# Optimization experiments

Measured on AMD Instinct MI355X. Metric: run time of the kernel, lower is better.

The kernel has to match this reference:

```python
import jax, jax.numpy as jnp
import numpy as np

H = 4096          # hidden_size
I = 11008         # intermediate_size
G = 128           # AWQ group_size
# AWQ interleaved nibble order within each packed int32
_ORDER = jnp.array([0, 4, 1, 5, 2, 6, 3, 7], dtype=jnp.int32) * 4


def _mk_lin(key, K, N):
    k1, k2, k3 = jax.random.split(key, 3)
    qw = jax.random.randint(k1, (K, N // 8), 0, 100, dtype=jnp.int32)
    qz = jax.random.randint(k2, (K // G, N // 8), 0, 100, dtype=jnp.int32)
    sc = jax.random.normal(k3, (K // G, N), dtype=jnp.float32) * 0.02
    return qw, qz, sc


def setup_inputs() -> dict:
    key = jax.random.key(0)
    ks = jax.random.split(key, 7)
    x = jax.random.normal(ks[0], (8, 16, H), dtype=jnp.float32)
    ln1_w = jnp.ones((H,), dtype=jnp.float32)
    ln2_w = jnp.ones((H,), dtype=jnp.float32)
    qkv_qw, qkv_qz, qkv_sc = _mk_lin(ks[1], H, 3 * H)
    o_qw, o_qz, o_sc = _mk_lin(ks[2], H, H)
    gu_qw, gu_qz, gu_sc = _mk_lin(ks[3], H, 2 * I)
    dn_qw, dn_qz, dn_sc = _mk_lin(ks[4], I, H)
    return dict(x=x, ln1_w=ln1_w, ln2_w=ln2_w,
                qkv_qw=qkv_qw, qkv_qz=qkv_qz, qkv_sc=qkv_sc,
                o_qw=o_qw, o_qz=o_qz, o_sc=o_sc,
                gu_qw=gu_qw, gu_qz=gu_qz, gu_sc=gu_sc,
                dn_qw=dn_qw, dn_qz=dn_qz, dn_sc=dn_sc)


def rmsnorm(x, w, eps=1e-6):
    return x * jax.lax.rsqrt(jnp.mean(x * x, axis=-1, keepdims=True) + eps) * w


def dequant(qw, qz, sc):
    # qw: [K, N//8] int32 -> [K, N]; qz: [K//G, N//8] -> [K//G, N]
    K = qw.shape[0]
    N = sc.shape[1]
    w = ((qw[:, :, None] >> _ORDER) & 0xF).reshape(K, N).astype(sc.dtype)
    z = ((qz[:, :, None] >> _ORDER) & 0xF).reshape(K // G, N).astype(sc.dtype)
    return (w - jnp.repeat(z, G, axis=0)) * jnp.repeat(sc, G, axis=0)


def lite_linear(x, qw, qz, sc):
    return x @ dequant(qw, qz, sc)


def reference(x, ln1_w, ln2_w,
              qkv_qw, qkv_qz, qkv_sc,
              o_qw, o_qz, o_sc,
              gu_qw, gu_qz, gu_sc,
              dn_qw, dn_qz, dn_sc):
    residual = x
    h = rmsnorm(x, ln1_w)
    h = lite_linear(h, qkv_qw, qkv_qz, qkv_sc)[..., :H]  # mock attn: take q slice
    h = lite_linear(h, o_qw, o_qz, o_sc)
    h = residual + h
    residual = h
    h = rmsnorm(h, ln2_w)
    gate_up = lite_linear(h, gu_qw, gu_qz, gu_sc)
    gate, up = gate_up[..., :I], gate_up[..., I:]
    h = lite_linear(jax.nn.silu(gate) * up, dn_qw, dn_qz, dn_sc)
    return residual + h
```

## Files before the change

kernel.cpp:

```cpp
#include <hip/hip_runtime.h>

typedef unsigned int   u32;
typedef unsigned short u16;

typedef _Float16 h2  __attribute__((ext_vector_type(2)));
typedef _Float16 h8  __attribute__((ext_vector_type(8)));
typedef float    f32x4 __attribute__((ext_vector_type(4)));

#define M_TOK 128

__device__ __forceinline__ u16 f2h_(float f) {
    _Float16 h = (_Float16)f; return __builtin_bit_cast(u16, h);
}
__device__ __forceinline__ float h2f_(u16 b) {
    _Float16 h = __builtin_bit_cast(_Float16, b); return (float)h;
}
__device__ __forceinline__ void acc8(uint4 v, float* s) {
#pragma unroll
    for (int i = 0; i < 4; ++i) {
        u32 w = ((const u32*)&v)[i];
        s[2 * i]     += h2f_((u16)(w & 0xFFFF));
        s[2 * i + 1] += h2f_((u16)(w >> 16));
    }
}

__constant__ int SHC[8] = {0, 16, 4, 20, 8, 24, 12, 28};

__launch_bounds__(256)
__global__ void pack_zs(const int* __restrict__ qz, const float* __restrict__ sc,
                        u32* __restrict__ zs, int qws, int scs, int Ncols, int total) {
    const int idx = blockIdx.x * 256 + threadIdx.x;
    if (idx >= total) return;
    const int g = idx / Ncols, n = idx - g * Ncols;
    const u32 d = (u32)qz[(size_t)g * qws + (n >> 3)];
    const u32 zj = (d >> SHC[n & 7]) & 15u;
    const u32 mz = 0xE400u | zj;
    const u16 sh = f2h_(sc[(size_t)g * scs + n]);
    zs[(size_t)g * Ncols + n] = mz | ((u32)sh << 16);
}


__launch_bounds__(256)
__global__ void rmsnorm_k(const float* __restrict__ in, const float* __restrict__ w,
                          u16* __restrict__ out) {
    const int row = blockIdx.x;
    const float* x = in + (size_t)row * 4096;
    float ss = 0.f;
#pragma unroll
    for (int j = 0; j < 16; ++j) {
        float v = x[threadIdx.x + 256 * j];
        ss += v * v;
    }
#pragma unroll
    for (int off = 32; off > 0; off >>= 1) ss += __shfl_down(ss, off, 64);
    __shared__ float ws4[4];
    if ((threadIdx.x & 63) == 0) ws4[threadIdx.x >> 6] = ss;
    __syncthreads();
    float total = ws4[0] + ws4[1] + ws4[2] + ws4[3];
    float r = rsqrtf(total * (1.f / 4096.f) + 1e-6f);
    const int mt = row >> 4, l16 = row & 15;
#pragma unroll
    for (int c2 = 0; c2 < 2; ++c2) {
        int c = threadIdx.x * 2 + c2;
        int kb = c >> 2, qq = c & 3;
        u16 o8[8];
#pragma unroll
        for (int j = 0; j < 8; ++j) {
            int i = c * 8 + j;
            o8[j] = f2h_(x[i] * r * w[i]);
        }
        *(uint4*)(out + ((size_t)(kb * 8 + mt) * 64 + qq * 16 + l16) * 8) = *(const uint4*)o8;
    }
}

template<int MSPLIT>
__launch_bounds__(256, MSPLIT == 2 ? 4 : 3)
__global__ void gemm_awq(const u16* __restrict__ A, const u32* __restrict__ zs,
                         const int* __restrict__ qw, u16* __restrict__ part,
                         int qws, int N, int K, int kchunk) {
    constexpr int MT = (MSPLIT == 2) ? 4 : 8;
    __shared__ __align__(16) char ldsB[4 * 9216];

    const int tid = threadIdx.x, w = tid >> 6, lane = tid & 63;
    const int q = lane >> 4, l16 = lane & 15;
    const int mh = (MSPLIT == 2) ? (w >> 1) : 0;
    const int nwg = gridDim.x, bid = blockIdx.x;
    const int qq8 = nwg >> 3, r8 = nwg & 7, xcd = bid & 7, boff = bid >> 3;
    const int bx = (xcd < r8 ? xcd * (qq8 + 1) : r8 * (qq8 + 1) + (xcd - r8) * qq8) + boff;
    const int n0w = (MSPLIT == 2) ? (bx * 64 + (w & 1) * 32) : (bx * 128 + w * 32);
    const int pc0 = n0w >> 3;
    const int kp = lane & 31, h = lane >> 5;
    const int sk = blockIdx.y, kc0 = sk * kchunk, kend = min(kc0 + kchunk, K);

    char* buf0 = ldsB + w * 9216;
    char* buf1 = buf0 + 4608;
    const u16* Ala = A + lane * 8;
    const int* qws_base = qw + pc0;
    const u32* zsA = zs + n0w + h * 8;
    const u32* zsB = zs + n0w + 16 + h * 8;

    f32x4 acc[MT][2] = {};
    uint4 za0, za1, zb0, zb1;

    auto ldraw = [&](int k0) -> uint4 {
        return *(const uint4*)(qws_base + (size_t)(k0 + lane) * qws);
    };
    auto loadzs = [&](int g) {
        za0 = *(const uint4*)(zsA + (size_t)g * N);
        za1 = *(const uint4*)(zsA + (size_t)g * N + 4);
        zb0 = *(const uint4*)(zsB + (size_t)g * N);
        zb1 = *(const uint4*)(zsB + (size_t)g * N + 4);
    };
    auto bperm8 = [&](uint4 rv, int* b) {
        const int i0 = kp * 8, i1 = i0 + 4;
        b[0] = __builtin_amdgcn_ds_bpermute(i0, (int)rv.x);
        b[1] = __builtin_amdgcn_ds_bpermute(i0, (int)rv.y);
        b[2] = __builtin_amdgcn_ds_bpermute(i0, (int)rv.z);
        b[3] = __builtin_amdgcn_ds_bpermute(i0, (int)rv.w);
        b[4] = __builtin_amdgcn_ds_bpermute(i1, (int)rv.x);
        b[5] = __builtin_amdgcn_ds_bpermute(i1, (int)rv.y);
        b[6] = __builtin_amdgcn_ds_bpermute(i1, (int)rv.z);
        b[7] = __builtin_amdgcn_ds_bpermute(i1, (int)rv.w);
    };
    auto emit_all = [&](const int* b, char* buf) {
        u32 qd0 = (u32)(h ? b[1] : b[0]);
        u32 qd1 = (u32)(h ? b[5] : b[4]);
        u32 qd2 = (u32)(h ? b[3] : b[2]);
        u32 qd3 = (u32)(h ? b[7] : b[6]);
        auto emit8 = [&](u32 w0, u32 w1, int nb, uint4 z0, uint4 z1) {
            char* bb = buf + kp * 4 + nb * 144;
            u32 w0s = w0 >> 4, w1s = w1 >> 4;
            auto em = [&](int j, u32 a0, u32 a1, int bsel, u32 zsj) {
                h2 mz = __builtin_bit_cast(h2, __builtin_amdgcn_perm(zsj, zsj, 0x01000100u));
                h2 s2 = __builtin_bit_cast(h2, __builtin_amdgcn_perm(zsj, zsj, 0x03020302u));
                u32 t = __builtin_amdgcn_perm(a1, a0, (u32)(bsel | ((bsel + 4) << 16)));
                u32 u = (t & 0x000F000Fu) | 0x64006400u;
                h2 v = (__builtin_bit_cast(h2, u) + mz) * s2;
                *(u32*)(bb + j * 144) = __builtin_bit_cast(u32, v);
            };
            em(0, w0, w1, 0, z0.x);  em(4, w0, w1, 1, z1.x);
            em(1, w0, w1, 2, z0.y);  em(5, w0, w1, 3, z1.y);
            em(2, w0s, w1s, 0, z0.z); em(6, w0s, w1s, 1, z1.z);
            em(3, w0s, w1s, 2, z0.w); em(7, w0s, w1s, 3, z1.w);
        };
        emit8(qd0, qd1, h * 8, za0, za1);
        emit8(qd2, qd3, 16 + h * 8, zb0, zb1);
    };

    loadzs(kc0 >> 7);
    uint4 rv0 = ldraw(kc0);
    uint4 rv_n = {0, 0, 0, 0}, rv_nn = {0, 0, 0, 0};
    if (kc0 + 64 < kend)  rv_n  = ldraw(kc0 + 64);
    if (kc0 + 128 < kend) rv_nn = ldraw(kc0 + 128);
    {
        int bp0[8];
        bperm8(rv0, bp0);
        emit_all(bp0, buf0);
    }
    if (((kc0 + 64) & 127) == 0 && kc0 + 64 < kend)
        loadzs((kc0 + 64) >> 7);

    char* cur = buf0; char* nxt = buf1;
    int bp[8];
    for (int k0 = kc0; k0 < kend; k0 += 64) {
        const bool kn1 = (k0 + 64) < kend, kn3 = (k0 + 192) < kend;
        uint4 bv[2][2];
#pragma unroll
        for (int c = 0; c < 2; ++c)
#pragma unroll
            for (int nt = 0; nt < 2; ++nt)
                bv[c][nt] = *(const uint4*)(cur + (nt * 16 + l16) * 144 + c * 64 + q * 16);
        if (kn1) bperm8(rv_n, bp);
        const int kb = k0 >> 5;
        __builtin_amdgcn_s_setprio(1);
#pragma unroll
        for (int c = 0; c < 2; ++c) {
            uint4 afc[MT];
#pragma unroll
            for (int mt = 0; mt < MT; ++mt)
                afc[mt] = *(const uint4*)(Ala + (size_t)((kb + c) * 8 + mh * MT + mt) * 512);
#pragma unroll
            for (int mt = 0; mt < MT; ++mt)
#pragma unroll
                for (int nt = 0; nt < 2; ++nt)
                    acc[mt][nt] = __builtin_amdgcn_mfma_f32_16x16x32_f16(
                        __builtin_bit_cast(h8, afc[mt]),
                        __builtin_bit_cast(h8, bv[c][nt]),
                        acc[mt][nt], 0, 0, 0);
        }
        __builtin_amdgcn_s_setprio(0);
        uint4 rv_f = {0, 0, 0, 0};
        if (kn3) rv_f = ldraw(k0 + 192);
        if (kn1) emit_all(bp, nxt);
        if (((k0 + 128) & 127) == 0 && (k0 + 128) < kend)
            loadzs((k0 + 128) >> 7);
        rv_n = rv_nn; rv_nn = rv_f;
        char* t = cur; cur = nxt; nxt = t;
    }

    u16* pp = part + (size_t)sk * M_TOK * N;
#pragma unroll
    for (int mt = 0; mt < MT; ++mt)
#pragma unroll
        for (int nt = 0; nt < 2; ++nt) {
            const int n = n0w + nt * 16 + l16;
#pragma unroll
            for (int r = 0; r < 4; ++r) {
                const int m = (mh * MT + mt) * 16 + q * 4 + r;
                pp[(size_t)m * N + n] = f2h_(acc[mt][nt][r]);
            }
        }
}

__launch_bounds__(256)
__global__ void reduce_to_afrag(const u16* __restrict__ part, u16* __restrict__ out,
                                int SK) {
    const int idx = blockIdx.x * 256 + threadIdx.x;
    const int m = idx >> 9, c = idx & 511;
    float s[8] = {};
    for (int k = 0; k < SK; ++k)
        acc8(*(const uint4*)(part + (size_t)k * 524288 + (size_t)m * 4096 + c * 8), s);
    const int kb = c >> 2, qq = c & 3, mt = m >> 4, l16 = m & 15;
    u16 o8[8];
#pragma unroll
    for (int j = 0; j < 8; ++j) o8[j] = f2h_(s[j]);
    *(uint4*)(out + ((size_t)(kb * 8 + mt) * 64 + qq * 16 + l16) * 8) = *(const uint4*)o8;
}

__launch_bounds__(256)
__global__ void reduce_add_f32(const u16* __restrict__ part, const float* __restrict__ resin,
                               float* __restrict__ out, int SK) {
    const int idx = blockIdx.x * 256 + threadIdx.x;
    const size_t base = (size_t)idx * 8;
    float s[8];
    *(float4*)&s[0] = *(const float4*)(resin + base);
    *(float4*)&s[4] = *(const float4*)(resin + base + 4);
    for (int k = 0; k < SK; ++k)
        acc8(*(const uint4*)(part + (size_t)k * 524288 + base), s);
    *(float4*)(out + base)     = *(const float4*)&s[0];
    *(float4*)(out + base + 4) = *(const float4*)&s[4];
}

__launch_bounds__(256)
__global__ void silu_mul(const u16* __restrict__ part, u16* __restrict__ act, int SK) {
    const int idx = blockIdx.x * 256 + threadIdx.x;
    const int m = idx / 1376, c = idx - m * 1376;
    const int nb = c * 8;
    float g[8] = {}, u[8] = {};
    for (int k = 0; k < SK; ++k) {
        const size_t base = (size_t)k * 2818048 + (size_t)m * 22016 + nb;
        acc8(*(const uint4*)(part + base), g);
        acc8(*(const uint4*)(part + base + 11008), u);
    }
    const int kb = nb >> 5, qq = (nb >> 3) & 3, mt = m >> 4, l16 = m & 15;
    u16 o8[8];
#pragma unroll
    for (int j = 0; j < 8; ++j) {
        float a = g[j] / (1.f + __expf(-g[j])) * u[j];
        o8[j] = f2h_(a);
    }
    *(uint4*)(act + ((size_t)(kb * 8 + mt) * 64 + qq * 16 + l16) * 8) = *(const uint4*)o8;
}

extern "C" void kernel_launch(void* const* d_in, const int* in_sizes, int n_in,
                              void* d_out, int out_size, void* d_ws, size_t ws_size,
                              hipStream_t stream) {
    const float* x      = (const float*)d_in[0];
    const float* ln1_w  = (const float*)d_in[1];
    const float* ln2_w  = (const float*)d_in[2];
    const int*   qkv_qw = (const int*)d_in[3];
    const int*   qkv_qz = (const int*)d_in[4];
    const float* qkv_sc = (const float*)d_in[5];
    const int*   o_qw   = (const int*)d_in[6];
    const int*   o_qz   = (const int*)d_in[7];
    const float* o_sc   = (const float*)d_in[8];
    const int*   gu_qw  = (const int*)d_in[9];
    const int*   gu_qz  = (const int*)d_in[10];
    const float* gu_sc  = (const float*)d_in[11];
    const int*   dn_qw  = (const int*)d_in[12];
    const int*   dn_qz  = (const int*)d_in[13];
    const float* dn_sc  = (const float*)d_in[14];
    float* out = (float*)d_out;

    char* ws = (char*)d_ws;
    u16*   pbuf = (u16*)(ws);
    u32*   zsb  = (u32*)(ws + 45088768);
    u16*   act  = (u16*)(ws + 47906816);
    float* res2 = (float*)(ws + 50724864);
    u16*   slot = (u16*)(ws + 52822016);

    rmsnorm_k<<<128, 256, 0, stream>>>(x, ln1_w, slot);
    pack_zs<<<512, 256, 0, stream>>>(qkv_qz, qkv_sc, zsb, 1536, 12288, 4096, 131072);

    gemm_awq<2><<<dim3(64, 16), 256, 0, stream>>>(slot, zsb, qkv_qw, pbuf,
                                                  1536, 4096, 4096, 256);
    reduce_to_afrag<<<256, 256, 0, stream>>>(pbuf, slot, 16);
    pack_zs<<<512, 256, 0, stream>>>(o_qz, o_sc, zsb, 512, 4096, 4096, 131072);

    gemm_awq<2><<<dim3(64, 16), 256, 0, stream>>>(slot, zsb, o_qw, pbuf,
                                                  512, 4096, 4096, 256);
    reduce_add_f32<<<256, 256, 0, stream>>>(pbuf, x, res2, 16);

    rmsnorm_k<<<128, 256, 0, stream>>>(res2, ln2_w, slot);
    pack_zs<<<2752, 256, 0, stream>>>(gu_qz, gu_sc, zsb, 2752, 22016, 22016, 704512);

    gemm_awq<1><<<dim3(172, 8), 256, 0, stream>>>(slot, zsb, gu_qw, pbuf,
                                                  2752, 22016, 4096, 512);
    silu_mul<<<688, 256, 0, stream>>>(pbuf, act, 8);
    pack_zs<<<1376, 256, 0, stream>>>(dn_qz, dn_sc, zsb, 512, 4096, 4096, 352256);

    gemm_awq<2><<<dim3(64, 20), 256, 0, stream>>>(act, zsb, dn_qw, pbuf,
                                                  512, 4096, 11008, 576);
    reduce_add_f32<<<256, 256, 0, stream>>>(pbuf, res2, out, 20);
}
```

Before: 318.7 us.

## Stage activation tiles in shared LDS and widen GEMM tiles to 128 columns

The GEMM kernel drops its MSPLIT template. Every wave now computes all 128 token rows over 32 columns, so each block covers 128 output columns. Activation fragments are cooperatively loaded into double-buffered shared LDS once per block rather than read from global by each wave, and block-wide barriers are added. The weight prefetch depth drops from two stages to one. Split-K factors and grid shapes are retuned for every projection. This cuts redundant global activation traffic, at the cost of a per-iteration __syncthreads, more LDS use (which lowers possible occupancy), and more accumulator registers for the small-N layers.

Measured after the change: 287.7 us. 1.11x faster.

```diff
diff --git a/kernel.cpp b/kernel.cpp
--- a/kernel.cpp
+++ b/kernel.cpp
@@ -73,33 +73,33 @@
     }
 }
 
-template<int MSPLIT>
-__launch_bounds__(256, MSPLIT == 2 ? 4 : 3)
+__launch_bounds__(256, 3)
 __global__ void gemm_awq(const u16* __restrict__ A, const u32* __restrict__ zs,
                          const int* __restrict__ qw, u16* __restrict__ part,
                          int qws, int N, int K, int kchunk) {
-    constexpr int MT = (MSPLIT == 2) ? 4 : 8;
-    __shared__ __align__(16) char ldsB[4 * 9216];
+    __shared__ __align__(16) char lds[51200];
 
     const int tid = threadIdx.x, w = tid >> 6, lane = tid & 63;
     const int q = lane >> 4, l16 = lane & 15;
-    const int mh = (MSPLIT == 2) ? (w >> 1) : 0;
     const int nwg = gridDim.x, bid = blockIdx.x;
     const int qq8 = nwg >> 3, r8 = nwg & 7, xcd = bid & 7, boff = bid >> 3;
     const int bx = (xcd < r8 ? xcd * (qq8 + 1) : r8 * (qq8 + 1) + (xcd - r8) * qq8) + boff;
-    const int n0w = (MSPLIT == 2) ? (bx * 64 + (w & 1) * 32) : (bx * 128 + w * 32);
+    const int n0w = bx * 128 + w * 32;
     const int pc0 = n0w >> 3;
     const int kp = lane & 31, h = lane >> 5;
     const int sk = blockIdx.y, kc0 = sk * kchunk, kend = min(kc0 + kchunk, K);
 
-    char* buf0 = ldsB + w * 9216;
-    char* buf1 = buf0 + 4608;
-    const u16* Ala = A + lane * 8;
+    char* ldsA0 = lds;
+    char* ldsA1 = lds + 16384;
+    char* myB   = lds + 32768 + w * 4608;
+    const char* Ab = (const char*)A;
+    const int stoff = w * 4096 + lane * 16;
+    const int aoff  = (q * 16 + l16) * 16;
     const int* qws_base = qw + pc0;
     const u32* zsA = zs + n0w + h * 8;
     const u32* zsB = zs + n0w + 16 + h * 8;
 
-    f32x4 acc[MT][2] = {};
+    f32x4 acc[8][2] = {};
     uint4 za0, za1, zb0, zb1;
 
     auto ldraw = [&](int k0) -> uint4 {
@@ -149,64 +149,102 @@
 
     loadzs(kc0 >> 7);
     uint4 rv0 = ldraw(kc0);
-    uint4 rv_n = {0, 0, 0, 0}, rv_nn = {0, 0, 0, 0};
-    if (kc0 + 64 < kend)  rv_n  = ldraw(kc0 + 64);
-    if (kc0 + 128 < kend) rv_nn = ldraw(kc0 + 128);
+    uint4 rv_n = {0, 0, 0, 0};
+    if (kc0 + 64 < kend) rv_n = ldraw(kc0 + 64);
+    {
+        const char* gs = Ab + (size_t)(kc0 >> 5) * 8192 + stoff;
+        uint4 s0 = *(const uint4*)(gs);
+        uint4 s1 = *(const uint4*)(gs + 1024);
+        uint4 s2 = *(const uint4*)(gs + 2048);
+        uint4 s3 = *(const uint4*)(gs + 3072);
+        *(uint4*)(ldsA0 + stoff)        = s0;
+        *(uint4*)(ldsA0 + stoff + 1024) = s1;
+        *(uint4*)(ldsA0 + stoff + 2048) = s2;
+        *(uint4*)(ldsA0 + stoff + 3072) = s3;
+    }
     {
         int bp0[8];
         bperm8(rv0, bp0);
-        emit_all(bp0, buf0);
+        emit_all(bp0, myB);
     }
     if (((kc0 + 64) & 127) == 0 && kc0 + 64 < kend)
         loadzs((kc0 + 64) >> 7);
-
-    char* cur = buf0; char* nxt = buf1;
+    __syncthreads();
+
+    char* cur = ldsA0; char* nxt = ldsA1;
     int bp[8];
     for (int k0 = kc0; k0 < kend; k0 += 64) {
-        const bool kn1 = (k0 + 64) < kend, kn3 = (k0 + 192) < kend;
-        uint4 bv[2][2];
-#pragma unroll
-        for (int c = 0; c < 2; ++c)
+        const bool kn1 = (k0 + 64) < kend, kn2 = (k0 + 128) < kend;
+        uint4 s0 = {0,0,0,0}, s1 = {0,0,0,0}, s2 = {0,0,0,0}, s3 = {0,0,0,0};
+        if (kn1) {
+            const char* gs = Ab + (size_t)((k0 + 64) >> 5) * 8192 + stoff;
+            s0 = *(const uint4*)(gs);
+            s1 = *(const uint4*)(gs + 1024);
+            s2 = *(const uint4*)(gs + 2048);
+            s3 = *(const uint4*)(gs + 3072);
+        }
+        uint4 rv_f = {0, 0, 0, 0};
+        if (kn2) rv_f = ldraw(k0 + 128);
+        {
+            uint4 bvc[2];
 #pragma unroll
             for (int nt = 0; nt < 2; ++nt)
-                bv[c][nt] = *(const uint4*)(cur + (nt * 16 + l16) * 144 + c * 64 + q * 16);
-        if (kn1) bperm8(rv_n, bp);
-        const int kb = k0 >> 5;
-        __builtin_amdgcn_s_setprio(1);
-#pragma unroll
-        for (int c = 0; c < 2; ++c) {
-            uint4 afc[MT];
-#pragma unroll
-            for (int mt = 0; mt < MT; ++mt)
-                afc[mt] = *(const uint4*)(Ala + (size_t)((kb + c) * 8 + mh * MT + mt) * 512);
-#pragma unroll
-            for (int mt = 0; mt < MT; ++mt)
+                bvc[nt] = *(const uint4*)(myB + (nt * 16 + l16) * 144 + q * 16);
+            uint4 afc[8];
+#pragma unroll
+            for (int mt = 0; mt < 8; ++mt)
+                afc[mt] = *(const uint4*)(cur + mt * 1024 + aoff);
+            if (kn1) bperm8(rv_n, bp);
+#pragma unroll
+            for (int mt = 0; mt < 8; ++mt)
 #pragma unroll
                 for (int nt = 0; nt < 2; ++nt)
                     acc[mt][nt] = __builtin_amdgcn_mfma_f32_16x16x32_f16(
                         __builtin_bit_cast(h8, afc[mt]),
-                        __builtin_bit_cast(h8, bv[c][nt]),
+                        __builtin_bit_cast(h8, bvc[nt]),
                         acc[mt][nt], 0, 0, 0);
         }
-        __builtin_amdgcn_s_setprio(0);
-        uint4 rv_f = {0, 0, 0, 0};
-        if (kn3) rv_f = ldraw(k0 + 192);
-        if (kn1) emit_all(bp, nxt);
+        {
+            uint4 bvc[2];
+#pragma unroll
+            for (int nt = 0; nt < 2; ++nt)
+                bvc[nt] = *(const uint4*)(myB + (nt * 16 + l16) * 144 + 64 + q * 16);
+            uint4 afc[8];
+#pragma unroll
+            for (int mt = 0; mt < 8; ++mt)
+                afc[mt] = *(const uint4*)(cur + 8192 + mt * 1024 + aoff);
+#pragma unroll
+            for (int mt = 0; mt < 8; ++mt)
+#pragma unroll
+                for (int nt = 0; nt < 2; ++nt)
+                    acc[mt][nt] = __builtin_amdgcn_mfma_f32_16x16x32_f16(
+                        __builtin_bit_cast(h8, afc[mt]),
+                        __builtin_bit_cast(h8, bvc[nt]),
+                        acc[mt][nt], 0, 0, 0);
+        }
+        if (kn1) {
+            emit_all(bp, myB);
+            *(uint4*)(nxt + stoff)        = s0;
+            *(uint4*)(nxt + stoff + 1024) = s1;
+            *(uint4*)(nxt + stoff + 2048) = s2;
+            *(uint4*)(nxt + stoff + 3072) = s3;
+        }
         if (((k0 + 128) & 127) == 0 && (k0 + 128) < kend)
             loadzs((k0 + 128) >> 7);
-        rv_n = rv_nn; rv_nn = rv_f;
+        __syncthreads();
+        rv_n = rv_f;
         char* t = cur; cur = nxt; nxt = t;
     }
 
     u16* pp = part + (size_t)sk * M_TOK * N;
 #pragma unroll
-    for (int mt = 0; mt < MT; ++mt)
+    for (int mt = 0; mt < 8; ++mt)
 #pragma unroll
         for (int nt = 0; nt < 2; ++nt) {
             const int n = n0w + nt * 16 + l16;
 #pragma unroll
             for (int r = 0; r < 4; ++r) {
-                const int m = (mh * MT + mt) * 16 + q * 4 + r;
+                const int m = mt * 16 + q * 4 + r;
                 pp[(size_t)m * N + n] = f2h_(acc[mt][nt][r]);
             }
         }
@@ -292,24 +330,24 @@
     rmsnorm_k<<<128, 256, 0, stream>>>(x, ln1_w, slot);
     pack_zs<<<512, 256, 0, stream>>>(qkv_qz, qkv_sc, zsb, 1536, 12288, 4096, 131072);
 
-    gemm_awq<2><<<dim3(64, 16), 256, 0, stream>>>(slot, zsb, qkv_qw, pbuf,
-                                                  1536, 4096, 4096, 256);
-    reduce_to_afrag<<<256, 256, 0, stream>>>(pbuf, slot, 16);
+    gemm_awq<<<dim3(32, 22), 256, 0, stream>>>(slot, zsb, qkv_qw, pbuf,
+                                               1536, 4096, 4096, 192);
+    reduce_to_afrag<<<256, 256, 0, stream>>>(pbuf, slot, 22);
     pack_zs<<<512, 256, 0, stream>>>(o_qz, o_sc, zsb, 512, 4096, 4096, 131072);
 
-    gemm_awq<2><<<dim3(64, 16), 256, 0, stream>>>(slot, zsb, o_qw, pbuf,
-                                                  512, 4096, 4096, 256);
-    reduce_add_f32<<<256, 256, 0, stream>>>(pbuf, x, res2, 16);
+    gemm_awq<<<dim3(32, 22), 256, 0, stream>>>(slot, zsb, o_qw, pbuf,
+                                               512, 4096, 4096, 192);
+    reduce_add_f32<<<256, 256, 0, stream>>>(pbuf, x, res2, 22);
 
     rmsnorm_k<<<128, 256, 0, stream>>>(res2, ln2_w, slot);
     pack_zs<<<2752, 256, 0, stream>>>(gu_qz, gu_sc, zsb, 2752, 22016, 22016, 704512);
 
-    gemm_awq<1><<<dim3(172, 8), 256, 0, stream>>>(slot, zsb, gu_qw, pbuf,
-                                                  2752, 22016, 4096, 512);
-    silu_mul<<<688, 256, 0, stream>>>(pbuf, act, 8);
+    gemm_awq<<<dim3(172, 5), 256, 0, stream>>>(slot, zsb, gu_qw, pbuf,
+                                               2752, 22016, 4096, 832);
+    silu_mul<<<688, 256, 0, stream>>>(pbuf, act, 5);
     pack_zs<<<1376, 256, 0, stream>>>(dn_qz, dn_sc, zsb, 512, 4096, 4096, 352256);
 
-    gemm_awq<2><<<dim3(64, 20), 256, 0, stream>>>(act, zsb, dn_qw, pbuf,
-                                                  512, 4096, 11008, 576);
-    reduce_add_f32<<<256, 256, 0, stream>>>(pbuf, res2, out, 20);
-}
+    gemm_awq<<<dim3(32, 25), 256, 0, stream>>>(act, zsb, dn_qw, pbuf,
+                                               512, 4096, 11008, 448);
+    reduce_add_f32<<<256, 256, 0, stream>>>(pbuf, res2, out, 25);
+}
```
